# Kernel optimization log

Hardware: AMD Instinct MI355X
Metric: run time of the kernel (lower is better)

## Reference

```python
import jax, jax.numpy as jnp
import numpy as np


def crf_log_likelihood(logits, tags, mask, transitions, start_trans, end_trans):
    """AllenNLP-style linear-chain CRF log-likelihood, summed over the batch.
    logits: [B,T,K] float, tags: [B,T] int, mask: [B,T] float (1=valid).
    include_start_end_transitions=True.
    """
    B, T, K = logits.shape
    lt = jnp.transpose(logits, (1, 0, 2))          # [T,B,K]
    mt = jnp.transpose(mask, (1, 0))               # [T,B]
    tt = jnp.transpose(tags, (1, 0))               # [T,B]

    # ---- partition function (forward algorithm) ----
    alpha0 = start_trans + lt[0]                   # [B,K]

    def part_step(alpha, xs):
        emit, m = xs                               # emit [B,K], m [B]
        # inner[b,i,j] = alpha[b,i] + transitions[i,j] + emit[b,j]
        inner = alpha[:, :, None] + emit[:, None, :] + transitions[None, :, :]
        new_alpha = jax.nn.logsumexp(inner, axis=1)
        alpha = new_alpha * m[:, None] + alpha * (1.0 - m[:, None])
        return alpha, None

    alpha, _ = jax.lax.scan(part_step, alpha0, (lt[1:], mt[1:]))
    log_denominator = jax.nn.logsumexp(alpha + end_trans, axis=1)  # [B]

    # ---- joint (gold-path) score ----
    score0 = start_trans[tt[0]]                    # [B]

    def joint_step(score, xs):
        cur, nxt, emit, m_cur, m_nxt = xs
        trans_s = transitions[cur, nxt]                                   # [B]
        emit_s = jnp.take_along_axis(emit, cur[:, None], axis=1)[:, 0]    # [B]
        return score + trans_s * m_nxt + emit_s * m_cur, None

    score, _ = jax.lax.scan(joint_step, score0,
                            (tt[:-1], tt[1:], lt[:-1], mt[:-1], mt[1:]))
    last_idx = (jnp.sum(mt, axis=0) - 1.0).astype(jnp.int32)              # [B]
    last_tags = tt[last_idx, jnp.arange(B)]                               # [B]
    last_emit = jnp.take_along_axis(lt[-1], last_tags[:, None], axis=1)[:, 0]
    score = score + end_trans[last_tags] + last_emit * mt[-1]
    return jnp.sum(score - log_denominator)


def setup_inputs() -> dict:
    key = jax.random.key(0)
    ks = jax.random.split(key, 6)
    B, T, D, K = 64, 512, 768, 21
    vectors = jax.random.normal(ks[0], (B, T, D), dtype=jnp.float32)
    targets = jax.random.randint(ks[1], (B, T), 0, K, dtype=jnp.int32)
    mask = jnp.ones((B, T), dtype=jnp.int32)
    # Linear(input_dim, n_classes)
    W = jax.random.normal(ks[2], (K, D), dtype=jnp.float32) * (1.0 / np.sqrt(D))
    b = jax.random.normal(ks[3], (K,), dtype=jnp.float32) * 0.01
    transitions = jax.random.normal(ks[4], (K, K), dtype=jnp.float32) * 0.1
    se = jax.random.normal(ks[5], (2, K), dtype=jnp.float32) * 0.1
    return {"vectors": vectors, "targets": targets, "mask": mask,
            "W": W, "b": b, "transitions": transitions,
            "start_trans": se[0], "end_trans": se[1]}


def reference(vectors, targets, mask, W, b, transitions, start_trans, end_trans):
    logits = jnp.einsum('btd,kd->btk', vectors, W) + b     # proj
    maskf = mask.astype(logits.dtype)
    ll = crf_log_likelihood(logits, targets, maskf, transitions, start_trans, end_trans)
    loss = -ll / jnp.sum(maskf)
    return loss, logits
```

## Files before the change

### kernel.cpp

```cpp
#include <hip/hip_runtime.h>

#define B_ 64
#define T_ 512
#define D_ 768
#define K_ 21
#define NCHUNK 32
#define CLEN 16
#define GSTRIDE 448
#define LOG21 3.0445224377234229965f
#define WSTRIDE 776
#define ASTRIDE 136

using f16x8 = __attribute__((ext_vector_type(8))) _Float16;
using h16x4 = __attribute__((ext_vector_type(4))) _Float16;
using f32x4 = __attribute__((ext_vector_type(4))) float;

__global__ __launch_bounds__(256) void proj_kernel(
    const float* __restrict__ A,
    const float* __restrict__ W,
    const float* __restrict__ bias,
    float* __restrict__ out)
{
    __shared__ _Float16 Wh[K_ * WSTRIDE];
    __shared__ _Float16 Ah[2][64 * ASTRIDE];
    const int tid  = threadIdx.x;
    const int lane = tid & 63;
    const int w    = tid >> 6;
    const int m    = lane & 15;
    const int quad = lane >> 4;
    const size_t row0 = (size_t)blockIdx.x * 64;

    {
        const float4* Wg = (const float4*)W;
        for (int i = tid; i < K_ * D_ / 4; i += 256) {
            const float4 v = Wg[i];
            const int fi = i * 4;
            const int r = fi / D_;
            const int c = fi - r * D_;
            h16x4 h;
            h[0] = (_Float16)v.x; h[1] = (_Float16)v.y;
            h[2] = (_Float16)v.z; h[3] = (_Float16)v.w;
            *(h16x4*)(&Wh[r * WSTRIDE + c]) = h;
        }
    }

    float4 pf[8];
    #pragma unroll
    for (int j = 0; j < 8; ++j) {
        const int i = tid + j * 256;
        const int r = i >> 5, c4 = i & 31;
        pf[j] = *(const float4*)(A + (row0 + r) * D_ + c4 * 4);
    }
    #pragma unroll
    for (int j = 0; j < 8; ++j) {
        const int i = tid + j * 256;
        const int r = i >> 5, c4 = i & 31;
        h16x4 h;
        h[0] = (_Float16)pf[j].x; h[1] = (_Float16)pf[j].y;
        h[2] = (_Float16)pf[j].z; h[3] = (_Float16)pf[j].w;
        *(h16x4*)(&Ah[0][r * ASTRIDE + c4 * 4]) = h;
    }
    __syncthreads();

    f32x4 acc0 = {0.f, 0.f, 0.f, 0.f};
    f32x4 acc1 = {0.f, 0.f, 0.f, 0.f};
    const int n1 = (16 + m < K_) ? 16 + m : K_ - 1;

    for (int kt = 0; kt < 6; ++kt) {
        if (kt < 5) {
            #pragma unroll
            for (int j = 0; j < 8; ++j) {
                const int i = tid + j * 256;
                const int r = i >> 5, c4 = i & 31;
                pf[j] = *(const float4*)(A + (row0 + r) * D_ + (kt + 1) * 128 + c4 * 4);
            }
        }
        const _Float16* Ab = Ah[kt & 1];
        #pragma unroll
        for (int s = 0; s < 4; ++s) {
            const f16x8 af = *(const f16x8*)(&Ab[(w * 16 + m) * ASTRIDE + s * 32 + quad * 8]);
            const f16x8 bf = *(const f16x8*)(&Wh[m * WSTRIDE + kt * 128 + s * 32 + quad * 8]);
            const f16x8 cf = *(const f16x8*)(&Wh[n1 * WSTRIDE + kt * 128 + s * 32 + quad * 8]);
            acc0 = __builtin_amdgcn_mfma_f32_16x16x32_f16(af, bf, acc0, 0, 0, 0);
            acc1 = __builtin_amdgcn_mfma_f32_16x16x32_f16(af, cf, acc1, 0, 0, 0);
        }
        if (kt < 5) {
            _Float16* Aw = Ah[(kt + 1) & 1];
            #pragma unroll
            for (int j = 0; j < 8; ++j) {
                const int i = tid + j * 256;
                const int r = i >> 5, c4 = i & 31;
                h16x4 h;
                h[0] = (_Float16)pf[j].x; h[1] = (_Float16)pf[j].y;
                h[2] = (_Float16)pf[j].z; h[3] = (_Float16)pf[j].w;
                *(h16x4*)(&Aw[r * ASTRIDE + c4 * 4]) = h;
            }
        }
        __syncthreads();
    }

    const size_t rbase = row0 + w * 16 + quad * 4;
    {
        const float bb = bias[m];
        float* o = out + 1 + rbase * K_ + m;
        #pragma unroll
        for (int r = 0; r < 4; ++r) o[(size_t)r * K_] = acc0[r] + bb;
    }
    const int col2 = 16 + m;
    if (col2 < K_) {
        const float bb = bias[col2];
        float* o = out + 1 + rbase * K_ + col2;
        #pragma unroll
        for (int r = 0; r < 4; ++r) o[(size_t)r * K_] = acc1[r] + bb;
    }
}

__global__ __launch_bounds__(64, 1) void chunk_kernel(
    const float* __restrict__ outF,
    const int*   __restrict__ mask,
    const float* __restrict__ trans,
    float* __restrict__ G,
    float* __restrict__ SC,
    int*   __restrict__ cnt)
{
    __shared__ float M0[441], M1[441];
    __shared__ float sET[441];
    __shared__ float em[CLEN * K_];
    __shared__ float smx[CLEN];
    __shared__ int   smask[CLEN];

    const int c = blockIdx.x;
    const int b = blockIdx.y;
    const int lane = threadIdx.x;
    if (c == 0 && b == 0 && lane == 0) *cnt = 0;
    const int t0 = c * CLEN + 1;
    const int nst = min(CLEN, T_ - t0);
    const int i_ = lane / 3;
    const int jg = lane - i_ * 3;
    const bool act = lane < 63;

    const float* lg = outF + 1 + (size_t)b * T_ * K_;
    for (int idx = lane; idx < nst * K_; idx += 64) em[idx] = lg[t0 * K_ + idx];
    if (lane < nst) smask[lane] = mask[b * T_ + t0 + lane];
    for (int idx = lane; idx < 441; idx += 64) {
        M0[idx] = (idx % 22 == 0) ? 1.0f : 0.0f;
        sET[idx] = __expf(trans[idx]);
    }
    __syncthreads();

    if (lane < nst) {
        float mx = -1e30f;
        for (int j = 0; j < K_; ++j) mx = fmaxf(mx, em[lane * K_ + j]);
        smx[lane] = mx;
    }
    __syncthreads();
    for (int idx = lane; idx < nst * K_; idx += 64)
        em[idx] = __expf(em[idx] - smx[idx / K_]) * (1.0f / 21.0f);

    float ETc[K_ * 7];
    if (act) {
        #pragma unroll
        for (int mm = 0; mm < K_; ++mm) {
            #pragma unroll
            for (int q = 0; q < 7; ++q)
                ETc[mm * 7 + q] = sET[mm * K_ + jg * 7 + q];
        }
    }
    __syncthreads();

    int cur = 0;
    for (int s = 0; s < nst; ++s) {
        if (smask[s] != 0) {
            const float* Mr = cur ? M1 : M0;
            float*       Mw = cur ? M0 : M1;
            float facc[7] = {0.f,0.f,0.f,0.f,0.f,0.f,0.f};
            if (act) {
                #pragma unroll
                for (int mm = 0; mm < K_; ++mm) {
                    const float lm = Mr[i_ * K_ + mm];
                    #pragma unroll
                    for (int q = 0; q < 7; ++q)
                        facc[q] = fmaf(lm, ETc[mm * 7 + q], facc[q]);
                }
            }
            __syncthreads();
            if (act) {
                #pragma unroll
                for (int q = 0; q < 7; ++q)
                    Mw[i_ * K_ + jg * 7 + q] = facc[q] * em[s * K_ + jg * 7 + q];
            }
            __syncthreads();
            cur ^= 1;
        }
    }

    float* Gc = G + (size_t)(b * NCHUNK + c) * GSTRIDE;
    const float* Mf = cur ? M1 : M0;
    for (int idx = lane; idx < 441; idx += 64) Gc[idx] = Mf[idx];
    if (lane == 0) {
        float sc = 0.0f;
        for (int s = 0; s < nst; ++s)
            if (smask[s] != 0) sc += smx[s] + LOG21;
        SC[b * NCHUNK + c] = sc;
    }
}

__global__ __launch_bounds__(256) void scan_fin_kernel(
    const float* __restrict__ outF,
    const int*   __restrict__ tags,
    const int*   __restrict__ mask,
    const float* __restrict__ trans,
    const float* __restrict__ startT,
    const float* __restrict__ endT,
    const float* __restrict__ G,
    const float* __restrict__ SC,
    float* __restrict__ ll,
    float* __restrict__ msum,
    int*   __restrict__ cnt,
    float* __restrict__ outW)
{
    __shared__ float sG[NCHUNK * GSTRIDE];
    __shared__ float sm[T_];
    __shared__ int   st[T_];
    __shared__ float part[8];
    __shared__ int   lastF;
    const int tid = threadIdx.x;
    const int lane = tid & 63;
    const int w = tid >> 6;
    const int b = blockIdx.x;
    const float* lg = outF + 1 + (size_t)b * T_ * K_;

    {
        const float4* Gf4 = (const float4*)(G + (size_t)b * NCHUNK * GSTRIDE);
        float4* dst = (float4*)sG;
        for (int i = tid; i < NCHUNK * GSTRIDE / 4; i += 256) dst[i] = Gf4[i];
    }
    for (int t = tid; t < T_; t += 256) {
        sm[t] = (float)mask[b * T_ + t];
        st[t] = tags[b * T_ + t];
    }
    __syncthreads();

    float logZ = 0.0f;
    if (w == 0) {
        const float scv = (lane < NCHUNK) ? SC[b * NCHUNK + lane] : 0.0f;
        const int jc = min(lane, K_ - 1);
        float v = (lane < K_) ? __expf(startT[lane] + lg[lane]) : 0.0f;
        float C = 0.0f;
        for (int c = 0; c < NCHUNK; ++c) {
            const float* Gc = sG + c * GSTRIDE;
            float a0 = 0.f, a1 = 0.f, a2 = 0.f;
            #pragma unroll
            for (int i = 0; i < K_; i += 3) {
                a0 = fmaf(__shfl(v, i,     64), Gc[i * K_ + jc],       a0);
                a1 = fmaf(__shfl(v, i + 1, 64), Gc[(i + 1) * K_ + jc], a1);
                a2 = fmaf(__shfl(v, i + 2, 64), Gc[(i + 2) * K_ + jc], a2);
            }
            const float s = a0 + a1 + a2;
            const float s0 = __shfl(s, 0, 64);
            v = s / s0;
            C += __logf(s0) + __shfl(scv, c, 64);
        }
        float term = (lane < K_) ? v * __expf(endT[lane]) : 0.0f;
        #pragma unroll
        for (int off = 16; off >= 1; off >>= 1) term += __shfl_xor(term, off, 64);
        term += __shfl_xor(term, 32, 64);
        logZ = C + __logf(term);
    } else {
        float sc = 0.0f, ms = 0.0f;
        for (int t = tid - 64; t < T_; t += 192) {
            const float mt = sm[t];
            ms += mt;
            if (t < T_ - 1) {
                const int ct = st[t], nt2 = st[t + 1];
                sc += trans[ct * K_ + nt2] * sm[t + 1] + lg[t * K_ + ct] * mt;
            }
        }
        #pragma unroll
        for (int off = 32; off >= 1; off >>= 1) {
            sc += __shfl_xor(sc, off, 64);
            ms += __shfl_xor(ms, off, 64);
        }
        if (lane == 0) { part[w] = sc; part[4 + w] = ms; }
    }
    __syncthreads();

    if (tid == 0) {
        float sc = part[1] + part[2] + part[3];
        float ms = part[5] + part[6] + part[7];
        const int lastIdx = (int)ms - 1;
        const int lastTag = st[lastIdx];
        sc += startT[st[0]] + endT[lastTag] + lg[(T_ - 1) * K_ + lastTag] * sm[T_ - 1];
        ll[b]   = sc - logZ;
        msum[b] = ms;
        __threadfence();
        lastF = (atomicAdd(cnt, 1) == B_ - 1) ? 1 : 0;
    }
    __syncthreads();

    if (lastF != 0 && w == 0) {
        __threadfence();
        float l  = ll[lane];
        float mm = msum[lane];
        #pragma unroll
        for (int off = 32; off >= 1; off >>= 1) {
            l  += __shfl_xor(l,  off, 64);
            mm += __shfl_xor(mm, off, 64);
        }
        if (lane == 0) outW[0] = -l / mm;
    }
}

__global__ __launch_bounds__(64) void fin_kernel(
    const float* __restrict__ ll, const float* __restrict__ msum,
    float* __restrict__ outF)
{
    const int lane = threadIdx.x;
    float l = ll[lane];
    float m = msum[lane];
    #pragma unroll
    for (int off = 32; off >= 1; off >>= 1) {
        l += __shfl_xor(l, off, 64);
        m += __shfl_xor(m, off, 64);
    }
    if (lane == 0) outF[0] = -l / m;
}

__global__ __launch_bounds__(64) void crf_kernel(
    const float* __restrict__ outF,
    const int*   __restrict__ tags,
    const int*   __restrict__ mask,
    const float* __restrict__ trans,
    const float* __restrict__ startT,
    const float* __restrict__ endT,
    float* __restrict__ ws)
{
    __shared__ float se[T_ * K_];
    __shared__ float sm[T_];
    __shared__ int   st[T_];
    const int b = blockIdx.x;
    const int lane = threadIdx.x;

    const float* lg = outF + 1 + (size_t)b * T_ * K_;
    for (int i = lane; i < T_ * K_; i += 64) se[i] = lg[i];
    for (int t = lane; t < T_; t += 64) {
        sm[t] = (float)mask[b * T_ + t];
        st[t] = tags[b * T_ + t];
    }
    __syncthreads();

    const int jc = lane < K_ ? lane : K_ - 1;
    float ET[K_];
    #pragma unroll
    for (int i = 0; i < K_; ++i) ET[i] = __expf(trans[i * K_ + jc]);

    float a0   = startT[jc] + se[jc];
    float r0   = __shfl(a0, 0, 64);
    float aRel = a0 - r0;
    float C    = r0;

    for (int t = 1; t < T_; ++t) {
        if (sm[t] != 0.0f) {
            float e = __expf(aRel);
            float s = 0.0f;
            #pragma unroll
            for (int i = 0; i < K_; ++i)
                s = fmaf(__shfl(e, i, 64), ET[i], s);
            float raw = __logf(s) + se[t * K_ + jc];
            float rr  = __shfl(raw, 0, 64);
            aRel = raw - rr;
            C   += rr;
        }
    }

    float contrib = (lane < K_) ? __expf(aRel + endT[jc]) : 0.0f;
    #pragma unroll
    for (int off = 32; off >= 1; off >>= 1) contrib += __shfl_xor(contrib, off, 64);
    const float logZ = C + __logf(contrib);

    float sc = 0.0f, ms = 0.0f;
    for (int t = lane; t < T_; t += 64) {
        const float mt = sm[t];
        ms += mt;
        if (t < T_ - 1) {
            const int ct = st[t], nt2 = st[t + 1];
            sc += trans[ct * K_ + nt2] * sm[t + 1] + se[t * K_ + ct] * mt;
        }
    }
    #pragma unroll
    for (int off = 32; off >= 1; off >>= 1) {
        sc += __shfl_xor(sc, off, 64);
        ms += __shfl_xor(ms, off, 64);
    }
    if (lane == 0) {
        const int lastIdx = (int)ms - 1;
        const int lastTag = st[lastIdx];
        sc += startT[st[0]] + endT[lastTag] + se[(T_ - 1) * K_ + lastTag] * sm[T_ - 1];
        ws[b]      = sc - logZ;
        ws[B_ + b] = ms;
    }
}

extern "C" void kernel_launch(void* const* d_in, const int* in_sizes, int n_in,
                              void* d_out, int out_size, void* d_ws, size_t ws_size,
                              hipStream_t stream) {
    const float* A     = (const float*)d_in[0];
    const int*   tags  = (const int*)  d_in[1];
    const int*   mask  = (const int*)  d_in[2];
    const float* W     = (const float*)d_in[3];
    const float* bias  = (const float*)d_in[4];
    const float* trans = (const float*)d_in[5];
    const float* stT   = (const float*)d_in[6];
    const float* enT   = (const float*)d_in[7];
    float* outF = (float*)d_out;
    float* ws   = (float*)d_ws;

    const size_t gFloats = (size_t)B_ * NCHUNK * GSTRIDE;
    const size_t scOff   = gFloats;
    const size_t llOff   = scOff + (size_t)B_ * NCHUNK;
    const size_t msOff   = llOff + B_;
    const size_t cntOff  = msOff + B_;
    const size_t needBytes = cntOff * sizeof(float) + sizeof(int);

    proj_kernel<<<512, 256, 0, stream>>>(A, W, bias, outF);

    if (ws_size >= needBytes) {
        float* G   = ws;
        float* SC  = ws + scOff;
        float* llp = ws + llOff;
        float* msv = ws + msOff;
        int*   cnt = (int*)(ws + cntOff);
        chunk_kernel<<<dim3(NCHUNK, B_), 64, 0, stream>>>(outF, mask, trans, G, SC, cnt);
        scan_fin_kernel<<<B_, 256, 0, stream>>>(outF, tags, mask, trans, stT, enT, G, SC, llp, msv, cnt, outF);
    } else {
        crf_kernel<<<B_, 64, 0, stream>>>(outF, tags, mask, trans, stT, enT, ws);
        fin_kernel<<<1, 64, 0, stream>>>(ws, ws + B_, outF);
    }
}
```

Measured before the change: 208.3 us.

## Load A fragments directly into MFMA registers, dropping LDS staging

The projection kernel stops staging the activation tile through double-buffered shared memory. Each lane now loads its own MFMA A-fragment straight from global memory into registers, converts it to fp16 there, and prefetches the next k-tile. This removes the per-iteration LDS writes and reads and the block-wide __syncthreads, and shrinks LDS so more blocks can fit per CU (launch bounds now request 4). In exchange, global loads are less coalesced: each lane reads 32-byte strided segments from rows 3 KB apart.

```diff
diff --git a/kernel.cpp b/kernel.cpp
--- a/kernel.cpp
+++ b/kernel.cpp
@@ -9,26 +9,33 @@
 #define GSTRIDE 448
 #define LOG21 3.0445224377234229965f
 #define WSTRIDE 776
-#define ASTRIDE 136
 
 using f16x8 = __attribute__((ext_vector_type(8))) _Float16;
 using h16x4 = __attribute__((ext_vector_type(4))) _Float16;
 using f32x4 = __attribute__((ext_vector_type(4))) float;
 
-__global__ __launch_bounds__(256) void proj_kernel(
+__global__ __launch_bounds__(256, 4) void proj_kernel(
     const float* __restrict__ A,
     const float* __restrict__ W,
     const float* __restrict__ bias,
     float* __restrict__ out)
 {
     __shared__ _Float16 Wh[K_ * WSTRIDE];
-    __shared__ _Float16 Ah[2][64 * ASTRIDE];
     const int tid  = threadIdx.x;
     const int lane = tid & 63;
     const int w    = tid >> 6;
     const int m    = lane & 15;
     const int quad = lane >> 4;
-    const size_t row0 = (size_t)blockIdx.x * 64;
+    const int gw   = blockIdx.x * 4 + w;
+    const float* Arow = A + ((size_t)gw * 16 + m) * D_;
+
+    float4 pf[8];
+    #pragma unroll
+    for (int j = 0; j < 8; ++j) {
+        const int s = j >> 1;
+        const int off = s * 32 + quad * 8 + (j & 1) * 4;
+        pf[j] = *(const float4*)(Arow + off);
+    }
 
     {
         const float4* Wg = (const float4*)W;
@@ -43,23 +50,6 @@
             *(h16x4*)(&Wh[r * WSTRIDE + c]) = h;
         }
     }
-
-    float4 pf[8];
-    #pragma unroll
-    for (int j = 0; j < 8; ++j) {
-        const int i = tid + j * 256;
-        const int r = i >> 5, c4 = i & 31;
-        pf[j] = *(const float4*)(A + (row0 + r) * D_ + c4 * 4);
-    }
-    #pragma unroll
-    for (int j = 0; j < 8; ++j) {
-        const int i = tid + j * 256;
-        const int r = i >> 5, c4 = i & 31;
-        h16x4 h;
-        h[0] = (_Float16)pf[j].x; h[1] = (_Float16)pf[j].y;
-        h[2] = (_Float16)pf[j].z; h[3] = (_Float16)pf[j].w;
-        *(h16x4*)(&Ah[0][r * ASTRIDE + c4 * 4]) = h;
-    }
     __syncthreads();
 
     f32x4 acc0 = {0.f, 0.f, 0.f, 0.f};
@@ -67,39 +57,36 @@
     const int n1 = (16 + m < K_) ? 16 + m : K_ - 1;
 
     for (int kt = 0; kt < 6; ++kt) {
+        f16x8 af[4];
+        #pragma unroll
+        for (int s = 0; s < 4; ++s) {
+            const float4 v0 = pf[2 * s], v1 = pf[2 * s + 1];
+            f16x8 a;
+            a[0] = (_Float16)v0.x; a[1] = (_Float16)v0.y;
+            a[2] = (_Float16)v0.z; a[3] = (_Float16)v0.w;
+            a[4] = (_Float16)v1.x; a[5] = (_Float16)v1.y;
+            a[6] = (_Float16)v1.z; a[7] = (_Float16)v1.w;
+            af[s] = a;
+        }
         if (kt < 5) {
+            const float* An = Arow + (kt + 1) * 128;
             #pragma unroll
             for (int j = 0; j < 8; ++j) {
-                const int i = tid + j * 256;
-                const int r = i >> 5, c4 = i & 31;
-                pf[j] = *(const float4*)(A + (row0 + r) * D_ + (kt + 1) * 128 + c4 * 4);
+                const int s = j >> 1;
+                const int off = s * 32 + quad * 8 + (j & 1) * 4;
+                pf[j] = *(const float4*)(An + off);
             }
         }
-        const _Float16* Ab = Ah[kt & 1];
         #pragma unroll
         for (int s = 0; s < 4; ++s) {
-            const f16x8 af = *(const f16x8*)(&Ab[(w * 16 + m) * ASTRIDE + s * 32 + quad * 8]);
-            const f16x8 bf = *(const f16x8*)(&Wh[m * WSTRIDE + kt * 128 + s * 32 + quad * 8]);
+            const f16x8 bf = *(const f16x8*)(&Wh[m  * WSTRIDE + kt * 128 + s * 32 + quad * 8]);
             const f16x8 cf = *(const f16x8*)(&Wh[n1 * WSTRIDE + kt * 128 + s * 32 + quad * 8]);
-            acc0 = __builtin_amdgcn_mfma_f32_16x16x32_f16(af, bf, acc0, 0, 0, 0);
-            acc1 = __builtin_amdgcn_mfma_f32_16x16x32_f16(af, cf, acc1, 0, 0, 0);
-        }
-        if (kt < 5) {
-            _Float16* Aw = Ah[(kt + 1) & 1];
-            #pragma unroll
-            for (int j = 0; j < 8; ++j) {
-                const int i = tid + j * 256;
-                const int r = i >> 5, c4 = i & 31;
-                h16x4 h;
-                h[0] = (_Float16)pf[j].x; h[1] = (_Float16)pf[j].y;
-                h[2] = (_Float16)pf[j].z; h[3] = (_Float16)pf[j].w;
-                *(h16x4*)(&Aw[r * ASTRIDE + c4 * 4]) = h;
-            }
-        }
-        __syncthreads();
-    }
-
-    const size_t rbase = row0 + w * 16 + quad * 4;
+            acc0 = __builtin_amdgcn_mfma_f32_16x16x32_f16(af[s], bf, acc0, 0, 0, 0);
+            acc1 = __builtin_amdgcn_mfma_f32_16x16x32_f16(af[s], cf, acc1, 0, 0, 0);
+        }
+    }
+
+    const size_t rbase = (size_t)gw * 16 + quad * 4;
     {
         const float bb = bias[m];
         float* o = out + 1 + rbase * K_ + m;
```

Result: no change. 209.5 us (+0.5%).
